# Performance work log

Measured on AMD Instinct MI355X. Metric: run time of the kernel, lower is better.

## Reference

```python
import jax, jax.numpy as jnp
import numpy as np

# NOTE: submodules (VecLayerNorm, VecLinear, VecActivation, VNAttention,
# VNCrossAttention, VNDynamicGraphAttention) are not in the provided source;
# they are reconstructed per standard Vector-Neuron (VN) equivariant layers.

B, C, NQ, NV, K, HEADS = 2, 128, 2048, 2048, 16, 8
HID = 4 * C
EPS = 1e-6
NS = 0.2  # LeakyReLU(0.2) slope used by VecActivation


def vec_layernorm(x, gamma, beta):
    # x: [B,C,3,N] -- equivariant LN: normalize per-channel vector norms,
    # LayerNorm the norms over the channel dim, rescale directions.
    n = jnp.sqrt(jnp.sum(x * x, axis=2, keepdims=True) + EPS)  # [B,C,1,N]
    mu = jnp.mean(n, axis=1, keepdims=True)
    var = jnp.var(n, axis=1, keepdims=True)
    ln = (n - mu) / jnp.sqrt(var + EPS) * gamma[None, :, None, None] + beta[None, :, None, None]
    return x / (n + EPS) * ln


def vlin(x, W):
    # VecLinear: bias-free linear over channel dim (equivariance). x: [B,C,3,N]
    return jnp.einsum('oc,bctn->botn', W, x)


def vn_attention(xq, xkv, Wq, Wk, Wv, Wo):
    # Global equivariant multi-head attention; scores from 3D-vector inner products.
    Bq, Cc, _, Nq = xq.shape
    Dh = Cc // HEADS
    q = vlin(xq, Wq).reshape(Bq, HEADS, Dh, 3, Nq)
    k = vlin(xkv, Wk).reshape(Bq, HEADS, Dh, 3, -1)
    vv = vlin(xkv, Wv).reshape(Bq, HEADS, Dh, 3, -1)
    s = jnp.einsum('bhdtn,bhdtm->bhnm', q, k) / np.float32(np.sqrt(3 * Dh))
    a = jax.nn.softmax(s, axis=-1)
    o = jnp.einsum('bhnm,bhdtm->bhdtn', a, vv).reshape(Bq, Cc, 3, Nq)
    return vlin(o, Wo)


def graph_attention(xq, xv, idx, We):
    # Local kNN graph attention: gather neighbor features by idx, build edge
    # features concat(v_j - q_i, q_i) -> VecLinear, softmax-weight over k neighbors.
    Bq, Cc, _, Nq = xq.shape
    vt = jnp.transpose(xv, (0, 3, 2, 1))                 # [B,Nv,3,C]
    nbr = jax.vmap(lambda vb, ib: vb[ib])(vt, idx)       # [B,Nq,k,3,C]
    qt = jnp.transpose(xq, (0, 3, 2, 1))                 # [B,Nq,3,C]
    center = qt[:, :, None, :, :]
    edge = jnp.concatenate([nbr - center, jnp.broadcast_to(center, nbr.shape)], axis=-1)  # [B,Nq,k,3,2C]
    feat = jnp.einsum('oc,bnktc->bnkto', We, edge)        # [B,Nq,k,3,C]
    s = jnp.einsum('bntc,bnktc->bnk', qt, nbr) / np.float32(np.sqrt(3 * Cc))
    a = jax.nn.softmax(s, axis=-1)
    out = jnp.einsum('bnk,bnkto->bnto', a, feat)          # [B,Nq,3,C]
    return jnp.transpose(out, (0, 3, 2, 1))               # [B,C,3,Nq]


def vn_leaky(x, D):
    # VN-LeakyReLU: learned direction d = D x; reflect negative half-space.
    d = vlin(x, D)
    dot = jnp.sum(x * d, axis=2, keepdims=True)
    dsq = jnp.sum(d * d, axis=2, keepdims=True)
    xneg = x - (dot / (dsq + EPS)) * d
    return NS * x + (1.0 - NS) * jnp.where(dot >= 0, x, xneg)


def setup_inputs() -> dict:
    key = jax.random.key(0)
    ks = jax.random.split(key, 24)

    def w(k_, o, i):
        return jax.random.normal(k_, (o, i), jnp.float32) / np.float32(np.sqrt(i))

    inp = {
        'q': jax.random.normal(ks[0], (B, C, 3, NQ), jnp.float32),
        'v': jax.random.normal(ks[1], (B, C, 3, NV), jnp.float32),
        'q_pos': jax.random.normal(ks[2], (B, NQ, 3), jnp.float32),
        'v_pos': jax.random.normal(ks[3], (B, NV, 3), jnp.float32),
        'self_attn_idx': jax.random.randint(ks[4], (B, NQ, K), 0, NQ),
        'cross_attn_idx': jax.random.randint(ks[5], (B, NQ, K), 0, NV),
        # VecLayerNorm affine params (norm1, norm2, norm_q, norm_v)
        'g1': jnp.ones((C,), jnp.float32), 'b1': jnp.zeros((C,), jnp.float32),
        'g2': jnp.ones((C,), jnp.float32), 'b2': jnp.zeros((C,), jnp.float32),
        'gq': jnp.ones((C,), jnp.float32), 'bq': jnp.zeros((C,), jnp.float32),
        'gv': jnp.ones((C,), jnp.float32), 'bv': jnp.zeros((C,), jnp.float32),
        # self attention (global VN attn + local graph attn + concat merge)
        'Wq_s': w(ks[6], C, C), 'Wk_s': w(ks[7], C, C), 'Wv_s': w(ks[8], C, C), 'Wo_s': w(ks[9], C, C),
        'We_s': w(ks[10], C, 2 * C), 'Wm_s': w(ks[11], C, 2 * C),
        # cross attention
        'Wq_c': w(ks[12], C, C), 'Wk_c': w(ks[13], C, C), 'Wv_c': w(ks[14], C, C), 'Wo_c': w(ks[15], C, C),
        'We_c': w(ks[16], C, 2 * C), 'Wm_c': w(ks[17], C, 2 * C),
        # MLP: VecLinear(C->4C) -> VN-LeakyReLU -> VecLinear(4C->C)
        'W1': w(ks[18], HID, C), 'Dact': w(ks[19], HID, HID), 'W2': w(ks[20], C, HID),
    }
    return inp


def reference(q, v, q_pos, v_pos, self_attn_idx, cross_attn_idx,
              g1, b1, g2, b2, gq, bq, gv, bv,
              Wq_s, Wk_s, Wv_s, Wo_s, We_s, Wm_s,
              Wq_c, Wk_c, Wv_c, Wo_c, We_c, Wm_c,
              W1, Dact, W2):
    # --- self-attention block (norm1 -> global attn + kNN graph attn -> merge -> residual)
    nx = vec_layernorm(q, g1, b1)
    f1 = vn_attention(nx, nx, Wq_s, Wk_s, Wv_s, Wo_s)
    f2 = graph_attention(nx, nx, self_attn_idx, We_s)
    q = q + vlin(jnp.concatenate([f1, f2], axis=1), Wm_s)
    # --- cross-attention block (norm_q / norm_v -> global cross attn + kNN cross graph attn -> merge -> residual)
    nq = vec_layernorm(q, gq, bq)
    nv = vec_layernorm(v, gv, bv)
    f1 = vn_attention(nq, nv, Wq_c, Wk_c, Wv_c, Wo_c)
    f2 = graph_attention(nq, nv, cross_attn_idx, We_c)
    q = q + vlin(jnp.concatenate([f1, f2], axis=1), Wm_c)
    # --- equivariant MLP (norm2 -> VecLinear -> VN-LeakyReLU -> VecLinear -> residual)
    nx = vec_layernorm(q, g2, b2)
    h = vn_leaky(vlin(nx, W1), Dact)
    q = q + vlin(h, W2)
    return q
```

## Files before the change

### kernel.cpp

```cpp
#include <hip/hip_runtime.h>
#include <math.h>

#define B_    2
#define C_    128
#define N_    2048
#define HID_  512
#define HEADS_ 8
#define EPS_  1e-6f
#define NS_   0.2f
#define KSPLIT 8

typedef __attribute__((ext_vector_type(8))) short short8v;
typedef __attribute__((ext_vector_type(4))) float f32x4;
typedef unsigned short ush;
typedef unsigned int u32;

__device__ inline ush f2bf(float f) {
    unsigned u = __float_as_uint(f);
    u += 0x7FFF + ((u >> 16) & 1);
    return (ush)(u >> 16);
}
__device__ inline float bf2f(ush u) { return __uint_as_float((u32)u << 16); }

__device__ inline u32 splitpack(float x) {
    ush hi = f2bf(x);
    float hf = __uint_as_float((u32)hi << 16);
    ush lo = f2bf(x - hf);
    return ((u32)hi << 16) | (u32)lo;
}

__device__ inline void unpack_hi(const u32* buf, short8v& h0, short8v& h1) {
    ush h[16];
    #pragma unroll
    for (int j = 0; j < 16; ++j) h[j] = (ush)(buf[j] >> 16);
    h0 = *(short8v*)&h[0]; h1 = *(short8v*)&h[8];
}

struct LNArgs {
    const float* x[2]; const float* g[2]; const float* bt[2]; ush* ysp[2];
};
__global__ __launch_bounds__(256) void ln_kernel(LNArgs a)
{
    __shared__ float norms[128][32];
    __shared__ float red1[8][32];
    __shared__ float red2[8][32];
    const int s = blockIdx.z;
    const float* x = a.x[s];
    const float* gma = a.g[s];
    const float* bta = a.bt[s];
    ush* ysp = a.ysp[s];

    const int b  = blockIdx.y;
    const int n0 = blockIdx.x * 32;
    const int nn = threadIdx.x & 31;
    const int cg = threadIdx.x >> 5;

    float s1 = 0.f, s2 = 0.f;
    for (int it = 0; it < 16; ++it) {
        int c = it * 8 + cg;
        size_t base = ((size_t)(b * C_ + c) * 3) * N_ + n0 + nn;
        float x0 = x[base], x1 = x[base + N_], x2 = x[base + 2 * N_];
        float nr = sqrtf(x0 * x0 + x1 * x1 + x2 * x2 + EPS_);
        norms[c][nn] = nr;
        s1 += nr; s2 += nr * nr;
    }
    red1[cg][nn] = s1; red2[cg][nn] = s2;
    __syncthreads();
    float S1 = 0.f, S2 = 0.f;
    #pragma unroll
    for (int g = 0; g < 8; ++g) { S1 += red1[g][nn]; S2 += red2[g][nn]; }
    float mu   = S1 * (1.f / 128.f);
    float var  = S2 * (1.f / 128.f) - mu * mu;
    float rstd = rsqrtf(var + EPS_);

    for (int it = 0; it < 16; ++it) {
        int c = it * 8 + cg;
        float nr = norms[c][nn];
        float ln = (nr - mu) * rstd * gma[c] + bta[c];
        float sc = ln / (nr + EPS_);
        size_t base = ((size_t)(b * C_ + c) * 3) * N_ + n0 + nn;
        ysp[base]          = f2bf(x[base] * sc);
        ysp[base + N_]     = f2bf(x[base + N_] * sc);
        ysp[base + 2 * N_] = f2bf(x[base + 2 * N_] * sc);
    }
}

struct WCArgs { const float* src[9]; u32* dst[9]; int n[9]; float scale[9]; };
__global__ __launch_bounds__(256) void wconv_kernel(WCArgs a)
{
    const int w = blockIdx.y;
    const int i = blockIdx.x * 256 + threadIdx.x;
    if (i < a.n[w]) a.dst[w][i] = splitpack(a.src[w][i] * a.scale[w]);
}

struct WFArgs {
    const float* Wm[2]; const float* Wo[2]; const float* We[2];
    u32* Wfa[2]; u32* Wfb[2];
};
__global__ __launch_bounds__(256) void wfuse_kernel(WFArgs a)
{
    const int tg = blockIdx.x * 256 + threadIdx.x;
    const int p = tg / 49152;
    const int rem = tg % 49152;
    if (rem < 16384) {
        const int o = rem >> 7, k = rem & 127;
        const float* Wm = a.Wm[p];
        const float* Wo = a.Wo[p];
        float acc = 0.f;
        #pragma unroll 4
        for (int c = 0; c < 128; ++c)
            acc += Wm[o * 256 + c] * Wo[c * 128 + k];
        a.Wfa[p][o * 128 + k] = splitpack(acc);
    } else {
        const int r2 = rem - 16384;
        const int o = r2 >> 8, k = r2 & 255;
        const float* Wm = a.Wm[p];
        const float* We = a.We[p];
        float acc = 0.f;
        #pragma unroll 4
        for (int c = 0; c < 128; ++c)
            acc += Wm[o * 256 + 128 + c] * We[c * 256 + k];
        a.Wfb[p][o * 256 + k] = splitpack(acc);
    }
}

template <int XMODE, int OMODE, bool XBF>
__device__ __forceinline__ void gemm_tile(
    const u32* __restrict__ Wsp, int wstride,
    const void* __restrict__ Xv, int K,
    const float* __restrict__ Z, float* __restrict__ Y,
    ush* __restrict__ Ybf, ush* __restrict__ Ytr,
    int b, int m0, int o0loc, int oglob, int Ostr,
    ush (*Wh)[64], ush (*Xh)[64])
{
    const int M = 3 * N_;
    const int tid = threadIdx.x;
    const int lane = tid & 63, wv = tid >> 6;
    const int col = lane & 15, grp = lane >> 4;
    const int wo = wv >> 1, wm = wv & 1;

    f32x4 acc[2][2];
    #pragma unroll
    for (int i = 0; i < 2; ++i)
        #pragma unroll
        for (int j = 0; j < 2; ++j) { f32x4 z = {0.f,0.f,0.f,0.f}; acc[i][j] = z; }

    for (int kk = 0; kk < K; kk += 64) {
        {
            const int o = tid >> 2, kg = tid & 3;
            const u32* src = Wsp + (size_t)(o0loc + o) * wstride + kk + kg * 16;
            u32 buf[16];
            #pragma unroll
            for (int j = 0; j < 4; ++j) *(uint4*)&buf[j * 4] = *(const uint4*)(src + j * 4);
            const int s0 = ((kg * 2)     ^ (o & 7)) << 3;
            const int s1 = ((kg * 2 + 1) ^ (o & 7)) << 3;
            short8v h0, h1; unpack_hi(buf, h0, h1);
            *(short8v*)&Wh[o][s0] = h0; *(short8v*)&Wh[o][s1] = h1;
        }
        if (XMODE == 0) {
            const int m = lane, kq = wv;
            const int s0 = ((kq * 2)     ^ (m & 7)) << 3;
            const int s1 = ((kq * 2 + 1) ^ (m & 7)) << 3;
            if (XBF) {
                const ush* src = (const ush*)Xv + ((size_t)b * K + kk + kq * 16) * M + m0 + m;
                ush h[16];
                #pragma unroll
                for (int j = 0; j < 16; ++j) h[j] = src[(size_t)j * M];
                *(short8v*)&Xh[m][s0] = *(short8v*)&h[0];
                *(short8v*)&Xh[m][s1] = *(short8v*)&h[8];
            } else {
                const u32* src = (const u32*)Xv + ((size_t)b * K + kk + kq * 16) * M + m0 + m;
                u32 buf[16];
                #pragma unroll
                for (int j = 0; j < 16; ++j) buf[j] = src[(size_t)j * M];
                short8v h0, h1; unpack_hi(buf, h0, h1);
                *(short8v*)&Xh[m][s0] = h0; *(short8v*)&Xh[m][s1] = h1;
            }
        } else {
            const int m = tid >> 2, kg = tid & 3;
            const int mg = m0 + m;
            const int n = mg & (N_ - 1), t = mg >> 11;
            const int s0 = ((kg * 2)     ^ (m & 7)) << 3;
            const int s1 = ((kg * 2 + 1) ^ (m & 7)) << 3;
            const ush* src = (const ush*)Xv + ((size_t)(b * N_ + n) * 3 + t) * K + kk + kg * 16;
            ush h[16];
            *(uint4*)&h[0] = *(const uint4*)(src);
            *(uint4*)&h[8] = *(const uint4*)(src + 8);
            *(short8v*)&Xh[m][s0] = *(short8v*)&h[0];
            *(short8v*)&Xh[m][s1] = *(short8v*)&h[8];
        }
        __syncthreads();
        #pragma unroll
        for (int kc = 0; kc < 2; ++kc) {
            const int sk = ((kc * 4 + grp) ^ (col & 7)) << 3;
            short8v ah0 = *(const short8v*)&Wh[wo * 32 + col][sk];
            short8v ah1 = *(const short8v*)&Wh[wo * 32 + 16 + col][sk];
            short8v xh0 = *(const short8v*)&Xh[wm * 32 + col][sk];
            short8v xh1 = *(const short8v*)&Xh[wm * 32 + 16 + col][sk];
            acc[0][0] = __builtin_amdgcn_mfma_f32_16x16x32_bf16(ah0, xh0, acc[0][0], 0, 0, 0);
            acc[0][1] = __builtin_amdgcn_mfma_f32_16x16x32_bf16(ah0, xh1, acc[0][1], 0, 0, 0);
            acc[1][0] = __builtin_amdgcn_mfma_f32_16x16x32_bf16(ah1, xh0, acc[1][0], 0, 0, 0);
            acc[1][1] = __builtin_amdgcn_mfma_f32_16x16x32_bf16(ah1, xh1, acc[1][1], 0, 0, 0);
        }
        __syncthreads();
    }
    #pragma unroll
    for (int of = 0; of < 2; ++of) {
        #pragma unroll
        for (int r = 0; r < 4; ++r) {
            const int o = oglob + wo * 32 + of * 16 + grp * 4 + r;
            #pragma unroll
            for (int mf = 0; mf < 2; ++mf) {
                const int mloc = m0 + wm * 32 + mf * 16 + col;
                const size_t idx = ((size_t)b * Ostr + o) * M + mloc;
                float v = acc[of][mf][r];
                if (OMODE == 0 || OMODE == 5) {
                    if (Z) v += Z[idx];
                    Y[idx] = v;
                }
                if (OMODE == 3 || OMODE == 5) Ybf[idx] = f2bf(v);
                if (OMODE == 4) {
                    ush bv = f2bf(v);
                    const int t = mloc >> 11, n = mloc & (N_ - 1);
                    const int h = (o >> 4) & 7, cl = o & 15;
                    const int d = cl * 3 + t;
                    if (o >= 256) {
                        const int kt = n >> 6, hh = (n >> 5) & 1, db = d >> 4;
                        const size_t idx2 = ((size_t)(b * 8 + h) * 192
                                           + (kt * 2 + hh) * 3 + db) * 512
                                          + (((n >> 3) & 3) * 16 + (d & 15)) * 8 + (n & 7);
                        Ybf[idx2] = bv;
                    } else {
                        const int isK = (o >> 7) & 1;
                        const int qg = n >> 4, half = d >> 5;
                        const size_t idx2 = ((size_t)(isK * 16 + b * 8 + h) * 256
                                           + qg * 2 + half) * 512
                                          + (((d >> 3) & 3) * 16 + (n & 15)) * 8 + (d & 7);
                        Ytr[idx2] = bv;
                    }
                }
            }
        }
    }
}

template <int XMODE, int OMODE, bool XBF>
__global__ __launch_bounds__(256) void gemm_kernel2(
    const u32* __restrict__ Wsp, int wstride,
    const void* __restrict__ Xv,
    const float* __restrict__ Z,
    float* __restrict__ Y, ush* __restrict__ Ybf,
    int Ostr, int obase, int K)
{
    __shared__ __align__(16) ush Wh[64][64];
    __shared__ __align__(16) ush Xh[64][64];
    gemm_tile<XMODE, OMODE, XBF>(Wsp, wstride, Xv, K, Z, Y, Ybf, nullptr,
                            blockIdx.z, blockIdx.x * 64,
                            blockIdx.y * 64, obase + blockIdx.y * 64, Ostr,
                            Wh, Xh);
}

__global__ __launch_bounds__(256) void wm2_kernel(
    const u32* __restrict__ Wfa, const u32* __restrict__ Wfb,
    const ush* __restrict__ ao, const ush* __restrict__ gb,
    const float* __restrict__ Z, float* __restrict__ Y)
{
    __shared__ __align__(16) ush Wh[64][64];
    __shared__ __align__(16) ush Xh[64][64];
    const int M = 3 * N_;
    const int b = blockIdx.z;
    const int m0 = blockIdx.x * 64;
    const int o0 = blockIdx.y * 64;
    const int tid = threadIdx.x;
    const int lane = tid & 63, wv = tid >> 6;
    const int col = lane & 15, grp = lane >> 4;
    const int wo = wv >> 1, wm = wv & 1;

    f32x4 acc[2][2];
    #pragma unroll
    for (int i = 0; i < 2; ++i)
        #pragma unroll
        for (int j = 0; j < 2; ++j) { f32x4 z = {0.f,0.f,0.f,0.f}; acc[i][j] = z; }

    for (int kk = 0; kk < 128; kk += 64) {
        {
            const int o = tid >> 2, kg = tid & 3;
            const u32* src = Wfa + (size_t)(o0 + o) * 128 + kk + kg * 16;
            u32 buf[16];
            #pragma unroll
            for (int j = 0; j < 4; ++j) *(uint4*)&buf[j * 4] = *(const uint4*)(src + j * 4);
            const int s0 = ((kg * 2)     ^ (o & 7)) << 3;
            const int s1 = ((kg * 2 + 1) ^ (o & 7)) << 3;
            short8v h0, h1; unpack_hi(buf, h0, h1);
            *(short8v*)&Wh[o][s0] = h0; *(short8v*)&Wh[o][s1] = h1;
        }
        {
            const int m = lane, kq = wv;
            const int s0 = ((kq * 2)     ^ (m & 7)) << 3;
            const int s1 = ((kq * 2 + 1) ^ (m & 7)) << 3;
            const ush* src = ao + ((size_t)b * 128 + kk + kq * 16) * M + m0 + m;
            ush h[16];
            #pragma unroll
            for (int j = 0; j < 16; ++j) h[j] = src[(size_t)j * M];
            *(short8v*)&Xh[m][s0] = *(short8v*)&h[0];
            *(short8v*)&Xh[m][s1] = *(short8v*)&h[8];
        }
        __syncthreads();
        #pragma unroll
        for (int kc = 0; kc < 2; ++kc) {
            const int sk = ((kc * 4 + grp) ^ (col & 7)) << 3;
            short8v ah0 = *(const short8v*)&Wh[wo * 32 + col][sk];
            short8v ah1 = *(const short8v*)&Wh[wo * 32 + 16 + col][sk];
            short8v xh0 = *(const short8v*)&Xh[wm * 32 + col][sk];
            short8v xh1 = *(const short8v*)&Xh[wm * 32 + 16 + col][sk];
            acc[0][0] = __builtin_amdgcn_mfma_f32_16x16x32_bf16(ah0, xh0, acc[0][0], 0, 0, 0);
            acc[0][1] = __builtin_amdgcn_mfma_f32_16x16x32_bf16(ah0, xh1, acc[0][1], 0, 0, 0);
            acc[1][0] = __builtin_amdgcn_mfma_f32_16x16x32_bf16(ah1, xh0, acc[1][0], 0, 0, 0);
            acc[1][1] = __builtin_amdgcn_mfma_f32_16x16x32_bf16(ah1, xh1, acc[1][1], 0, 0, 0);
        }
        __syncthreads();
    }

    for (int kk = 0; kk < 256; kk += 64) {
        {
            const int o = tid >> 2, kg = tid & 3;
            const u32* src = Wfb + (size_t)(o0 + o) * 256 + kk + kg * 16;
            u32 buf[16];
            #pragma unroll
            for (int j = 0; j < 4; ++j) *(uint4*)&buf[j * 4] = *(const uint4*)(src + j * 4);
            const int s0 = ((kg * 2)     ^ (o & 7)) << 3;
            const int s1 = ((kg * 2 + 1) ^ (o & 7)) << 3;
            short8v h0, h1; unpack_hi(buf, h0, h1);
            *(short8v*)&Wh[o][s0] = h0; *(short8v*)&Wh[o][s1] = h1;
        }
        {
            const int m = tid >> 2, kg = tid & 3;
            const int mg = m0 + m;
            const int n = mg & (N_ - 1), t = mg >> 11;
            const int s0 = ((kg * 2)     ^ (m & 7)) << 3;
            const int s1 = ((kg * 2 + 1) ^ (m & 7)) << 3;
            const ush* src = gb + ((size_t)(b * N_ + n) * 3 + t) * 256 + kk + kg * 16;
            ush h[16];
            *(uint4*)&h[0] = *(const uint4*)(src);
            *(uint4*)&h[8] = *(const uint4*)(src + 8);
            *(short8v*)&Xh[m][s0] = *(short8v*)&h[0];
            *(short8v*)&Xh[m][s1] = *(short8v*)&h[8];
        }
        __syncthreads();
        #pragma unroll
        for (int kc = 0; kc < 2; ++kc) {
            const int sk = ((kc * 4 + grp) ^ (col & 7)) << 3;
            short8v ah0 = *(const short8v*)&Wh[wo * 32 + col][sk];
            short8v ah1 = *(const short8v*)&Wh[wo * 32 + 16 + col][sk];
            short8v xh0 = *(const short8v*)&Xh[wm * 32 + col][sk];
            short8v xh1 = *(const short8v*)&Xh[wm * 32 + 16 + col][sk];
            acc[0][0] = __builtin_amdgcn_mfma_f32_16x16x32_bf16(ah0, xh0, acc[0][0], 0, 0, 0);
            acc[0][1] = __builtin_amdgcn_mfma_f32_16x16x32_bf16(ah0, xh1, acc[0][1], 0, 0, 0);
            acc[1][0] = __builtin_amdgcn_mfma_f32_16x16x32_bf16(ah1, xh0, acc[1][0], 0, 0, 0);
            acc[1][1] = __builtin_amdgcn_mfma_f32_16x16x32_bf16(ah1, xh1, acc[1][1], 0, 0, 0);
        }
        __syncthreads();
    }

    #pragma unroll
    for (int of = 0; of < 2; ++of) {
        #pragma unroll
        for (int r = 0; r < 4; ++r) {
            const int o = o0 + wo * 32 + of * 16 + grp * 4 + r;
            #pragma unroll
            for (int mf = 0; mf < 2; ++mf) {
                const int mloc = m0 + wm * 32 + mf * 16 + col;
                const size_t idx = ((size_t)b * 128 + o) * M + mloc;
                Y[idx] = acc[of][mf][r] + Z[idx];
            }
        }
    }
}

struct QKVArgs {
    const u32* W0; const u32* W1; const u32* W2;
    const ush* X0; const ush* X1; const ush* X2;
};

__global__ __launch_bounds__(256) void qkv_tr_kernel(QKVArgs A,
        ush* __restrict__ vfm, ush* __restrict__ qktb,
        const ush* __restrict__ ts0, ush* __restrict__ td0,
        const ush* __restrict__ ts1, ush* __restrict__ td1)
{
    __shared__ __align__(16) ush Wh[64][64];
    __shared__ __align__(16) ush Xh[64][64];
    __shared__ ush ttile[32][34];
    const int bx = blockIdx.x;
    if (bx < 1152) {
        const int z = bx / 576, rem = bx % 576;
        const int y = rem / 96, x = rem % 96;
        const int wi = y >> 1;
        const u32* W = wi == 0 ? A.W0 : (wi == 1 ? A.W1 : A.W2);
        const ush* X = wi == 0 ? A.X0 : (wi == 1 ? A.X1 : A.X2);
        gemm_tile<0, 4, true>(W, 128, X, 128, nullptr, nullptr, vfm, qktb,
                        z, x * 64, (y & 1) * 64, y * 64, 384,
                        Wh, Xh);
    } else {
        int i = bx - 1152;
        const int which = i / 1536; i %= 1536;
        const ush* src = which ? ts1 : ts0;
        ush* dst = which ? td1 : td0;
        const int x = i & 63, y = (i >> 6) & 3, z = i >> 8;
        const int b = z / 3, t = z % 3;
        const int n0 = x * 32, c0 = y * 32;
        const int tx = threadIdx.x & 31, ty = threadIdx.x >> 5;
        #pragma unroll
        for (int p = 0; p < 4; ++p) {
            int c = c0 + ty + p * 8;
            ttile[ty + p * 8][tx] = src[((size_t)(b * C_ + c) * 3 + t) * N_ + n0 + tx];
        }
        __syncthreads();
        #pragma unroll
        for (int p = 0; p < 4; ++p) {
            int n = n0 + ty + p * 8;
            dst[((size_t)(b * N_ + n) * 3 + t) * C_ + c0 + tx] = ttile[tx][ty + p * 8];
        }
    }
}

__global__ __launch_bounds__(256) void attn_mfma_kernel(
    const ush* __restrict__ vfm, const ush* __restrict__ qktb,
    ush* __restrict__ pacc, float* __restrict__ pml)
{
    __shared__ __align__(16) ush Pl[4][2][16][64];

    const int flat = blockIdx.x;
    const int xcd  = flat & 7;
    const int slot = flat >> 3;
    const int gid  = xcd * 4 + (slot >> 6);
    const int q32  = slot & 63;
    const int bh   = gid & 15;
    const int zz   = gid >> 4;

    const int tid = threadIdx.x;
    const int lane = tid & 63, wv = tid >> 6;
    const int col = lane & 15, grp = lane >> 4;
    const int c7  = col & 7;
    const int kz  = zz * 4 + wv;
    const int ks0 = kz * (N_ / KSPLIT);

    const ush* Qpl = qktb + (size_t)bh * 131072;
    const ush* Kpl = qktb + (size_t)(16 + bh) * 131072;
    const ush* Vpl = vfm  + (size_t)bh * 98304;

    short8v qf[2][2];
    #pragma unroll
    for (int qi = 0; qi < 2; ++qi) {
        const int qg = q32 * 2 + qi;
        qf[qi][0] = *(const short8v*)(Qpl + ((size_t)qg * 2 + 0) * 512 + lane * 8);
        qf[qi][1] = *(const short8v*)(Qpl + ((size_t)qg * 2 + 1) * 512 + lane * 8);
    }

    f32x4 acc[2][3];
    #pragma unroll
    for (int qi = 0; qi < 2; ++qi)
        #pragma unroll
        for (int db = 0; db < 3; ++db) { f32x4 z = {0.f,0.f,0.f,0.f}; acc[qi][db] = z; }
    float m_i[2] = {0.f, 0.f};
    float l_l[2] = {0.f, 0.f};

    const int NT = (N_ / KSPLIT) / 64;
    for (int mt = 0; mt < NT; ++mt) {
        const int m0 = ks0 + mt * 64;

        short8v ka[4][2];
        #pragma unroll
        for (int kb = 0; kb < 4; ++kb) {
            const size_t kg = (m0 >> 4) + kb;
            ka[kb][0] = *(const short8v*)(Kpl + (kg * 2 + 0) * 512 + lane * 8);
            ka[kb][1] = *(const short8v*)(Kpl + (kg * 2 + 1) * 512 + lane * 8);
        }
        const int kt = m0 >> 6;
        short8v vf[2][3];
        #pragma unroll
        for (int hh = 0; hh < 2; ++hh)
            #pragma unroll
            for (int db = 0; db < 3; ++db)
                vf[hh][db] = *(const short8v*)(Vpl + (size_t)((kt * 2 + hh) * 3 + db) * 512 + lane * 8);

        f32x4 sf[2][4];
        __builtin_amdgcn_s_setprio(1);
        #pragma unroll
        for (int qi = 0; qi < 2; ++qi)
            #pragma unroll
            for (int kb = 0; kb < 4; ++kb) {
                f32x4 z = {0.f, 0.f, 0.f, 0.f};
                z = __builtin_amdgcn_mfma_f32_16x16x32_bf16(ka[kb][0], qf[qi][0], z, 0, 0, 0);
                z = __builtin_amdgcn_mfma_f32_16x16x32_bf16(ka[kb][1], qf[qi][1], z, 0, 0, 0);
                sf[qi][kb] = z;
            }
        __builtin_amdgcn_s_setprio(0);

        #pragma unroll
        for (int qi = 0; qi < 2; ++qi) {
            float psum = 0.f;
            #pragma unroll
            for (int kb = 0; kb < 4; ++kb) {
                float e0 = __expf(sf[qi][kb][0] - m_i[qi]);
                float e1 = __expf(sf[qi][kb][1] - m_i[qi]);
                float e2 = __expf(sf[qi][kb][2] - m_i[qi]);
                float e3 = __expf(sf[qi][kb][3] - m_i[qi]);
                psum += (e0 + e1) + (e2 + e3);
                u32 r0, r1;
                asm("v_cvt_pk_bf16_f32 %0, %1, %2" : "=v"(r0) : "v"(e0), "v"(e1));
                asm("v_cvt_pk_bf16_f32 %0, %1, %2" : "=v"(r1) : "v"(e2), "v"(e3));
                const int un = (4 * kb + grp) ^ (c7 << 1);
                uint2 pk2; pk2.x = r0; pk2.y = r1;
                *(uint2*)&Pl[wv][qi][col][un << 2] = pk2;
            }
            l_l[qi] += psum;
        }

        __builtin_amdgcn_s_setprio(1);
        #pragma unroll
        for (int qi = 0; qi < 2; ++qi)
            #pragma unroll
            for (int hh = 0; hh < 2; ++hh) {
                const int ur = (8 * hh + 2 * grp) ^ (c7 << 1);
                short8v pf = *(const short8v*)&Pl[wv][qi][col][ur << 2];
                #pragma unroll
                for (int db = 0; db < 3; ++db)
                    acc[qi][db] = __builtin_amdgcn_mfma_f32_16x16x32_bf16(vf[hh][db], pf, acc[qi][db], 0, 0, 0);
            }
        __builtin_amdgcn_s_setprio(0);

        #pragma unroll
        for (int qi = 0; qi < 2; ++qi) {
            float pmax = -1e30f;
            #pragma unroll
            for (int kb = 0; kb < 4; ++kb)
                #pragma unroll
                for (int r = 0; r < 4; ++r) pmax = fmaxf(pmax, sf[qi][kb][r]);
            pmax = fmaxf(pmax, __shfl_xor(pmax, 16, 64));
            pmax = fmaxf(pmax, __shfl_xor(pmax, 32, 64));
            if (!__all(pmax - m_i[qi] <= 8.0f)) {
                float mnew = fmaxf(m_i[qi], pmax);
                float sc = __expf(m_i[qi] - mnew);
                l_l[qi] *= sc;
                #pragma unroll
                for (int db = 0; db < 3; ++db) {
                    acc[qi][db][0] *= sc; acc[qi][db][1] *= sc;
                    acc[qi][db][2] *= sc; acc[qi][db][3] *= sc;
                }
                m_i[qi] = mnew;
            }
        }
    }

    const int ntile = q32 >> 1, qh = q32 & 1;
    const size_t pb = (size_t)(kz * 16 + bh) * 32 + ntile;
    #pragma unroll
    for (int qi = 0; qi < 2; ++qi) {
        float l = l_l[qi];
        l += __shfl_xor(l, 16, 64);
        l += __shfl_xor(l, 32, 64);
        const int q = qh * 32 + qi * 16 + col;
        #pragma unroll
        for (int db = 0; db < 3; ++db)
            #pragma unroll
            for (int r = 0; r < 4; ++r) {
                int d = db * 16 + grp * 4 + r;
                pacc[pb * 3072 + d * 64 + q] = f2bf(acc[qi][db][r]);
            }
        if (grp == 0) {
            pml[pb * 128 + q]      = m_i[qi];
            pml[pb * 128 + 64 + q] = l;
        }
    }
}

__global__ __launch_bounds__(256) void graph_kernel(
    const ush* __restrict__ tq, const ush* __restrict__ tv,
    const int* __restrict__ idx, ush* __restrict__ gbuf)
{
    __shared__ float centerf[384];
    __shared__ ush nbr_l[16][384];
    __shared__ float sd[16];
    __shared__ int nbr_i[16];
    const int b = blockIdx.y, n = blockIdx.x;
    const int tid = threadIdx.x;
    const ush* qrow = tq + (size_t)(b * N_ + n) * 384;
    for (int e = tid; e < 384; e += 256) centerf[e] = bf2f(qrow[e]);
    if (tid < 16) nbr_i[tid] = idx[(size_t)(b * N_ + n) * 16 + tid];
    __syncthreads();

    const int lane = tid & 63, wv = tid >> 6;
    for (int kk = 0; kk < 4; ++kk) {
        int k = wv * 4 + kk;
        const u32* vrow = (const u32*)(tv + ((size_t)b * N_ + nbr_i[k]) * 384);
        float p = 0.f;
        #pragma unroll
        for (int jj = 0; jj < 3; ++jj) {
            int e2 = lane + jj * 64;
            u32 v2 = vrow[e2];
            ((u32*)nbr_l[k])[e2] = v2;
            p += centerf[e2 * 2]     * bf2f((ush)(v2 & 0xffff))
               + centerf[e2 * 2 + 1] * bf2f((ush)(v2 >> 16));
        }
        #pragma unroll
        for (int off = 32; off; off >>= 1) p += __shfl_down(p, off, 64);
        if (lane == 0) sd[k] = p * 0.05103103630798288f;
    }
    __syncthreads();

    float mx = -1e30f;
    #pragma unroll
    for (int k = 0; k < 16; ++k) mx = fmaxf(mx, sd[k]);
    float a[16]; float ssum = 0.f;
    #pragma unroll
    for (int k = 0; k < 16; ++k) { a[k] = __expf(sd[k] - mx); ssum += a[k]; }
    float inv = 1.f / ssum;

    for (int e = tid; e < 384; e += 256) {
        float accv = 0.f;
        #pragma unroll
        for (int k = 0; k < 16; ++k)
            accv += a[k] * bf2f(nbr_l[k][e]);
        accv *= inv;
        float ce = centerf[e];
        int t = e >> 7, c = e & 127;
        size_t gb = ((size_t)(b * N_ + n) * 3 + t) * 256;
        gbuf[gb + c]       = f2bf(accv - ce);
        gbuf[gb + 128 + c] = f2bf(ce);
    }
}

__global__ __launch_bounds__(256) void attn_reduce_kernel(
    const ush* __restrict__ pacc, const float* __restrict__ pml,
    ush* __restrict__ ao)
{
    const int nt = blockIdx.x, bh = blockIdx.y;
    const int b = bh >> 3, h = bh & 7;
    const int tid = threadIdx.x;
    const int q = tid & 63, dg = tid >> 6;

    size_t pb[KSPLIT];
    float m[KSPLIT], l[KSPLIT];
    #pragma unroll
    for (int kz = 0; kz < KSPLIT; ++kz) {
        pb[kz] = (size_t)(kz * 16 + bh) * 32 + nt;
        m[kz] = pml[pb[kz] * 128 + q];
        l[kz] = pml[pb[kz] * 128 + 64 + q];
    }
    float ms = -1e30f;
    #pragma unroll
    for (int kz = 0; kz < KSPLIT; ++kz) ms = fmaxf(ms, m[kz]);
    float w[KSPLIT], ls = 0.f;
    #pragma unroll
    for (int kz = 0; kz < KSPLIT; ++kz) { w[kz] = __expf(m[kz] - ms); ls += l[kz] * w[kz]; }
    const float inv = 1.f / ls;

    const size_t hb = ((size_t)(b * C_ + h * 16)) * 3 * N_;
    #pragma unroll
    for (int j = 0; j < 12; ++j) {
        int d = dg * 12 + j;
        float o = 0.f;
        #pragma unroll
        for (int kz = 0; kz < KSPLIT; ++kz)
            o += bf2f(pacc[pb[kz] * 3072 + d * 64 + q]) * w[kz];
        ao[hb + (size_t)d * N_ + nt * 64 + q] = f2bf(o * inv);
    }
}

__global__ __launch_bounds__(256) void leaky_kernel(const float* __restrict__ x,
                                                    const float* __restrict__ d,
                                                    ush* __restrict__ y)
{
    size_t p = (size_t)blockIdx.x * 256 + threadIdx.x;
    size_t bh = p / N_, n = p % N_;
    size_t base = bh * 3 * N_ + n;
    float x0 = x[base], x1 = x[base + N_], x2 = x[base + 2 * N_];
    float d0 = d[base], d1 = d[base + N_], d2 = d[base + 2 * N_];
    float dot = x0 * d0 + x1 * d1 + x2 * d2;
    float dsq = d0 * d0 + d1 * d1 + d2 * d2;
    float f = dot / (dsq + EPS_);
    bool pos = dot >= 0.f;
    float y0 = pos ? x0 : x0 - f * d0;
    float y1 = pos ? x1 : x1 - f * d1;
    float y2 = pos ? x2 : x2 - f * d2;
    y[base]          = f2bf(NS_ * x0 + (1.f - NS_) * y0);
    y[base + N_]     = f2bf(NS_ * x1 + (1.f - NS_) * y1);
    y[base + 2 * N_] = f2bf(NS_ * x2 + (1.f - NS_) * y2);
}

extern "C" void kernel_launch(void* const* d_in, const int* in_sizes, int n_in,
                              void* d_out, int out_size, void* d_ws, size_t ws_size,
                              hipStream_t stream)
{
    const float* q_in = (const float*)d_in[0];
    const float* v_in = (const float*)d_in[1];
    const int*   idx_s = (const int*)d_in[4];
    const int*   idx_c = (const int*)d_in[5];
    const float* g1 = (const float*)d_in[6];
    const float* b1 = (const float*)d_in[7];
    const float* g2 = (const float*)d_in[8];
    const float* b2 = (const float*)d_in[9];
    const float* gq = (const float*)d_in[10];
    const float* bq = (const float*)d_in[11];
    const float* gv = (const float*)d_in[12];
    const float* bv = (const float*)d_in[13];
    float* out = (float*)d_out;
    float* ws  = (float*)d_ws;

    const size_t S1 = (size_t)B_ * C_ * 3 * N_;
    ush*   nx_b  = (ush*)(ws + 2*S1);
    ush*   nv_b  = (ush*)(ws + 3*S1);
    ush*   vfm   = (ush*)(ws + 4*S1);
    ush*   qktb  = (ush*)(ws + 5*S1) + S1;
    ush*   ao_b  = (ush*)(ws + 7*S1);
    ush*   gbuf_b= (ush*)(ws + 8*S1);
    float* qa    = ws + 12*S1;
    float* qb    = ws + 13*S1;
    ush*   t1_b  = (ush*)(ws + 14*S1);
    ush*   t2_b  = (ush*)(ws + 15*S1);
    u32*   wsp   = (u32*)(ws + 16*S1);
    ush*   pacc  = (ush*)(ws + 8*S1);
    float* pml   = (float*)(ws + 2*S1);
    float* hd    = ws;
    float* h1    = ws + 4*S1;
    ush*   h1_b  = (ush*)(ws + 14*S1);
    ush*   h1_b2 = (ush*)(ws + 8*S1);

    const int wn[9]   = {16384,16384,16384, 16384,16384,16384, 65536,262144,65536};
    const int wsrc[9] = {14,15,16, 20,21,22, 26,27,28};
    u32* wd[9];
    {
        int off = 0;
        for (int i = 0; i < 9; ++i) { wd[i] = wsp + off; off += wn[i]; }
    }
    u32 *Wq_s = wd[0], *Wk_s = wd[1], *Wv_s = wd[2];
    u32 *Wq_c = wd[3], *Wk_c = wd[4], *Wv_c = wd[5];
    u32 *W1 = wd[6], *Dact = wd[7], *W2 = wd[8];
    u32* Wfa_s = wsp + 491520;
    u32* Wfb_s = Wfa_s + 16384;
    u32* Wfa_c = Wfb_s + 32768;
    u32* Wfb_c = Wfa_c + 16384;

    hipMemsetAsync(qktb, 0, (size_t)32 * 131072 * sizeof(ush), stream);

    {
        WCArgs a;
        for (int i = 0; i < 9; ++i) {
            a.src[i] = (const float*)d_in[wsrc[i]];
            a.dst[i] = wd[i];
            a.n[i]   = wn[i];
            a.scale[i] = 1.f;
        }
        a.scale[0] = 0.14433756729740643f;
        a.scale[3] = 0.14433756729740643f;
        wconv_kernel<<<dim3(1024, 9), 256, 0, stream>>>(a);
    }
    {
        WFArgs a;
        a.Wm[0] = (const float*)d_in[19]; a.Wo[0] = (const float*)d_in[17]; a.We[0] = (const float*)d_in[18];
        a.Wm[1] = (const float*)d_in[25]; a.Wo[1] = (const float*)d_in[23]; a.We[1] = (const float*)d_in[24];
        a.Wfa[0] = Wfa_s; a.Wfb[0] = Wfb_s;
        a.Wfa[1] = Wfa_c; a.Wfb[1] = Wfb_c;
        wfuse_kernel<<<dim3(384), 256, 0, stream>>>(a);
    }

    dim3 gar(N_ / 64, B_ * HEADS_);
    dim3 ggr(N_, B_);
    dim3 gwm(96, 2, B_);
    dim3 gg512(96, 8, B_);

    {
        LNArgs la{};
        la.x[0] = q_in; la.g[0] = g1; la.bt[0] = b1; la.ysp[0] = nx_b;
        ln_kernel<<<dim3(64, B_, 1), 256, 0, stream>>>(la);
    }
    {
        QKVArgs A{Wq_s, Wk_s, Wv_s, nx_b, nx_b, nx_b};
        qkv_tr_kernel<<<dim3(1152 + 1536), 256, 0, stream>>>(A, vfm, qktb, nx_b, t1_b, nullptr, nullptr);
    }
    attn_mfma_kernel<<<dim3(2048), 256, 0, stream>>>(vfm, qktb, pacc, pml);
    attn_reduce_kernel<<<gar, 256, 0, stream>>>(pacc, pml, ao_b);
    graph_kernel<<<ggr, 256, 0, stream>>>(t1_b, t1_b, idx_s, gbuf_b);
    wm2_kernel<<<gwm, 256, 0, stream>>>(Wfa_s, Wfb_s, ao_b, gbuf_b, q_in, qa);

    {
        LNArgs la{};
        la.x[0] = qa;   la.g[0] = gq; la.bt[0] = bq; la.ysp[0] = nx_b;
        la.x[1] = v_in; la.g[1] = gv; la.bt[1] = bv; la.ysp[1] = nv_b;
        ln_kernel<<<dim3(64, B_, 2), 256, 0, stream>>>(la);
    }
    {
        QKVArgs A{Wq_c, Wk_c, Wv_c, nx_b, nv_b, nv_b};
        qkv_tr_kernel<<<dim3(1152 + 3072), 256, 0, stream>>>(A, vfm, qktb, nx_b, t1_b, nv_b, t2_b);
    }
    attn_mfma_kernel<<<dim3(2048), 256, 0, stream>>>(vfm, qktb, pacc, pml);
    attn_reduce_kernel<<<gar, 256, 0, stream>>>(pacc, pml, ao_b);
    graph_kernel<<<ggr, 256, 0, stream>>>(t1_b, t2_b, idx_c, gbuf_b);
    wm2_kernel<<<gwm, 256, 0, stream>>>(Wfa_c, Wfb_c, ao_b, gbuf_b, qa, qb);

    {
        LNArgs la{};
        la.x[0] = qb; la.g[0] = g2; la.bt[0] = b2; la.ysp[0] = nx_b;
        ln_kernel<<<dim3(64, B_, 1), 256, 0, stream>>>(la);
    }
    gemm_kernel2<0,5,true><<<gg512, 256, 0, stream>>>(W1, 128, nx_b, nullptr, h1, h1_b, 512, 0, 128);
    gemm_kernel2<0,0,true><<<gg512, 256, 0, stream>>>(Dact, 512, h1_b, nullptr, hd, nullptr, 512, 0, 512);
    leaky_kernel<<<dim3((B_ * HID_ * N_) / 256), 256, 0, stream>>>(h1, hd, h1_b2);
    gemm_kernel2<0,0,true><<<dim3(96, 2, B_), 256, 0, stream>>>(W2, 512, h1_b2, qb, out, nullptr, 128, 0, 512);
}
```

Before: 251.6 us.

## Merge attention reduce with graph attention kernel; store MLP intermediates in bf16

Merges the split-K attention reduction and the kNN graph attention into one launch. The first 512 blocks do the reduction and the remaining 4096 blocks do the graph gather, which removes one launch per block and lets the two independent jobs overlap. The MLP's W1 and Dact GEMM outputs are now written only as bf16, so the fp32 copies are gone and the leaky activation reads bf16 inputs, cutting memory traffic. Workspace buffers are reassigned to match (gbuf moves to offset 0, hd_b to 1*S1). The cost is slightly lower precision for the inputs to the activation.

```diff
diff --git a/kernel.cpp b/kernel.cpp
--- a/kernel.cpp
+++ b/kernel.cpp
@@ -214,11 +214,11 @@
                 const int mloc = m0 + wm * 32 + mf * 16 + col;
                 const size_t idx = ((size_t)b * Ostr + o) * M + mloc;
                 float v = acc[of][mf][r];
-                if (OMODE == 0 || OMODE == 5) {
+                if (OMODE == 0) {
                     if (Z) v += Z[idx];
                     Y[idx] = v;
                 }
-                if (OMODE == 3 || OMODE == 5) Ybf[idx] = f2bf(v);
+                if (OMODE == 3) Ybf[idx] = f2bf(v);
                 if (OMODE == 4) {
                     ush bv = f2bf(v);
                     const int t = mloc >> 11, n = mloc & (N_ - 1);
@@ -574,7 +574,9 @@
     }
 }
 
-__global__ __launch_bounds__(256) void graph_kernel(
+__global__ __launch_bounds__(256) void reduce_graph_kernel(
+    const ush* __restrict__ pacc, const float* __restrict__ pml,
+    ush* __restrict__ ao,
     const ush* __restrict__ tq, const ush* __restrict__ tv,
     const int* __restrict__ idx, ush* __restrict__ gbuf)
 {
@@ -582,100 +584,98 @@
     __shared__ ush nbr_l[16][384];
     __shared__ float sd[16];
     __shared__ int nbr_i[16];
-    const int b = blockIdx.y, n = blockIdx.x;
     const int tid = threadIdx.x;
-    const ush* qrow = tq + (size_t)(b * N_ + n) * 384;
-    for (int e = tid; e < 384; e += 256) centerf[e] = bf2f(qrow[e]);
-    if (tid < 16) nbr_i[tid] = idx[(size_t)(b * N_ + n) * 16 + tid];
-    __syncthreads();
-
-    const int lane = tid & 63, wv = tid >> 6;
-    for (int kk = 0; kk < 4; ++kk) {
-        int k = wv * 4 + kk;
-        const u32* vrow = (const u32*)(tv + ((size_t)b * N_ + nbr_i[k]) * 384);
-        float p = 0.f;
-        #pragma unroll
-        for (int jj = 0; jj < 3; ++jj) {
-            int e2 = lane + jj * 64;
-            u32 v2 = vrow[e2];
-            ((u32*)nbr_l[k])[e2] = v2;
-            p += centerf[e2 * 2]     * bf2f((ush)(v2 & 0xffff))
-               + centerf[e2 * 2 + 1] * bf2f((ush)(v2 >> 16));
-        }
-        #pragma unroll
-        for (int off = 32; off; off >>= 1) p += __shfl_down(p, off, 64);
-        if (lane == 0) sd[k] = p * 0.05103103630798288f;
-    }
-    __syncthreads();
-
-    float mx = -1e30f;
-    #pragma unroll
-    for (int k = 0; k < 16; ++k) mx = fmaxf(mx, sd[k]);
-    float a[16]; float ssum = 0.f;
-    #pragma unroll
-    for (int k = 0; k < 16; ++k) { a[k] = __expf(sd[k] - mx); ssum += a[k]; }
-    float inv = 1.f / ssum;
-
-    for (int e = tid; e < 384; e += 256) {
-        float accv = 0.f;
-        #pragma unroll
-        for (int k = 0; k < 16; ++k)
-            accv += a[k] * bf2f(nbr_l[k][e]);
-        accv *= inv;
-        float ce = centerf[e];
-        int t = e >> 7, c = e & 127;
-        size_t gb = ((size_t)(b * N_ + n) * 3 + t) * 256;
-        gbuf[gb + c]       = f2bf(accv - ce);
-        gbuf[gb + 128 + c] = f2bf(ce);
-    }
-}
-
-__global__ __launch_bounds__(256) void attn_reduce_kernel(
-    const ush* __restrict__ pacc, const float* __restrict__ pml,
-    ush* __restrict__ ao)
-{
-    const int nt = blockIdx.x, bh = blockIdx.y;
-    const int b = bh >> 3, h = bh & 7;
-    const int tid = threadIdx.x;
-    const int q = tid & 63, dg = tid >> 6;
-
-    size_t pb[KSPLIT];
-    float m[KSPLIT], l[KSPLIT];
-    #pragma unroll
-    for (int kz = 0; kz < KSPLIT; ++kz) {
-        pb[kz] = (size_t)(kz * 16 + bh) * 32 + nt;
-        m[kz] = pml[pb[kz] * 128 + q];
-        l[kz] = pml[pb[kz] * 128 + 64 + q];
-    }
-    float ms = -1e30f;
-    #pragma unroll
-    for (int kz = 0; kz < KSPLIT; ++kz) ms = fmaxf(ms, m[kz]);
-    float w[KSPLIT], ls = 0.f;
-    #pragma unroll
-    for (int kz = 0; kz < KSPLIT; ++kz) { w[kz] = __expf(m[kz] - ms); ls += l[kz] * w[kz]; }
-    const float inv = 1.f / ls;
-
-    const size_t hb = ((size_t)(b * C_ + h * 16)) * 3 * N_;
-    #pragma unroll
-    for (int j = 0; j < 12; ++j) {
-        int d = dg * 12 + j;
-        float o = 0.f;
-        #pragma unroll
-        for (int kz = 0; kz < KSPLIT; ++kz)
-            o += bf2f(pacc[pb[kz] * 3072 + d * 64 + q]) * w[kz];
-        ao[hb + (size_t)d * N_ + nt * 64 + q] = f2bf(o * inv);
-    }
-}
-
-__global__ __launch_bounds__(256) void leaky_kernel(const float* __restrict__ x,
-                                                    const float* __restrict__ d,
+
+    if (blockIdx.x < 512) {
+        const int nt = blockIdx.x & 31, bh = blockIdx.x >> 5;
+        const int b = bh >> 3, h = bh & 7;
+        const int q = tid & 63, dg = tid >> 6;
+
+        size_t pb[KSPLIT];
+        float m[KSPLIT], l[KSPLIT];
+        #pragma unroll
+        for (int kz = 0; kz < KSPLIT; ++kz) {
+            pb[kz] = (size_t)(kz * 16 + bh) * 32 + nt;
+            m[kz] = pml[pb[kz] * 128 + q];
+            l[kz] = pml[pb[kz] * 128 + 64 + q];
+        }
+        float ms = -1e30f;
+        #pragma unroll
+        for (int kz = 0; kz < KSPLIT; ++kz) ms = fmaxf(ms, m[kz]);
+        float w[KSPLIT], ls = 0.f;
+        #pragma unroll
+        for (int kz = 0; kz < KSPLIT; ++kz) { w[kz] = __expf(m[kz] - ms); ls += l[kz] * w[kz]; }
+        const float inv = 1.f / ls;
+
+        const size_t hb = ((size_t)(b * C_ + h * 16)) * 3 * N_;
+        #pragma unroll
+        for (int j = 0; j < 12; ++j) {
+            int d = dg * 12 + j;
+            float o = 0.f;
+            #pragma unroll
+            for (int kz = 0; kz < KSPLIT; ++kz)
+                o += bf2f(pacc[pb[kz] * 3072 + d * 64 + q]) * w[kz];
+            ao[hb + (size_t)d * N_ + nt * 64 + q] = f2bf(o * inv);
+        }
+    } else {
+        const int j = blockIdx.x - 512;
+        const int b = j >> 11, n = j & 2047;
+        const ush* qrow = tq + (size_t)(b * N_ + n) * 384;
+        for (int e = tid; e < 384; e += 256) centerf[e] = bf2f(qrow[e]);
+        if (tid < 16) nbr_i[tid] = idx[(size_t)(b * N_ + n) * 16 + tid];
+        __syncthreads();
+
+        const int lane = tid & 63, wv = tid >> 6;
+        for (int kk = 0; kk < 4; ++kk) {
+            int k = wv * 4 + kk;
+            const u32* vrow = (const u32*)(tv + ((size_t)b * N_ + nbr_i[k]) * 384);
+            float p = 0.f;
+            #pragma unroll
+            for (int jj = 0; jj < 3; ++jj) {
+                int e2 = lane + jj * 64;
+                u32 v2 = vrow[e2];
+                ((u32*)nbr_l[k])[e2] = v2;
+                p += centerf[e2 * 2]     * bf2f((ush)(v2 & 0xffff))
+                   + centerf[e2 * 2 + 1] * bf2f((ush)(v2 >> 16));
+            }
+            #pragma unroll
+            for (int off = 32; off; off >>= 1) p += __shfl_down(p, off, 64);
+            if (lane == 0) sd[k] = p * 0.05103103630798288f;
+        }
+        __syncthreads();
+
+        float mx = -1e30f;
+        #pragma unroll
+        for (int k = 0; k < 16; ++k) mx = fmaxf(mx, sd[k]);
+        float a[16]; float ssum = 0.f;
+        #pragma unroll
+        for (int k = 0; k < 16; ++k) { a[k] = __expf(sd[k] - mx); ssum += a[k]; }
+        float inv = 1.f / ssum;
+
+        for (int e = tid; e < 384; e += 256) {
+            float accv = 0.f;
+            #pragma unroll
+            for (int k = 0; k < 16; ++k)
+                accv += a[k] * bf2f(nbr_l[k][e]);
+            accv *= inv;
+            float ce = centerf[e];
+            int t = e >> 7, c = e & 127;
+            size_t gb = ((size_t)(b * N_ + n) * 3 + t) * 256;
+            gbuf[gb + c]       = f2bf(accv - ce);
+            gbuf[gb + 128 + c] = f2bf(ce);
+        }
+    }
+}
+
+__global__ __launch_bounds__(256) void leaky_kernel(const ush* __restrict__ x,
+                                                    const ush* __restrict__ d,
                                                     ush* __restrict__ y)
 {
     size_t p = (size_t)blockIdx.x * 256 + threadIdx.x;
     size_t bh = p / N_, n = p % N_;
     size_t base = bh * 3 * N_ + n;
-    float x0 = x[base], x1 = x[base + N_], x2 = x[base + 2 * N_];
-    float d0 = d[base], d1 = d[base + N_], d2 = d[base + 2 * N_];
+    float x0 = bf2f(x[base]), x1 = bf2f(x[base + N_]), x2 = bf2f(x[base + 2 * N_]);
+    float d0 = bf2f(d[base]), d1 = bf2f(d[base + N_]), d2 = bf2f(d[base + 2 * N_]);
     float dot = x0 * d0 + x1 * d1 + x2 * d2;
     float dsq = d0 * d0 + d1 * d1 + d2 * d2;
     float f = dot / (dsq + EPS_);
@@ -708,12 +708,12 @@
     float* ws  = (float*)d_ws;
 
     const size_t S1 = (size_t)B_ * C_ * 3 * N_;
+    ush*   gbuf_b= (ush*)(ws);
     ush*   nx_b  = (ush*)(ws + 2*S1);
     ush*   nv_b  = (ush*)(ws + 3*S1);
     ush*   vfm   = (ush*)(ws + 4*S1);
     ush*   qktb  = (ush*)(ws + 5*S1) + S1;
     ush*   ao_b  = (ush*)(ws + 7*S1);
-    ush*   gbuf_b= (ush*)(ws + 8*S1);
     float* qa    = ws + 12*S1;
     float* qb    = ws + 13*S1;
     ush*   t1_b  = (ush*)(ws + 14*S1);
@@ -721,8 +721,7 @@
     u32*   wsp   = (u32*)(ws + 16*S1);
     ush*   pacc  = (ush*)(ws + 8*S1);
     float* pml   = (float*)(ws + 2*S1);
-    float* hd    = ws;
-    float* h1    = ws + 4*S1;
+    ush*   hd_b  = (ush*)(ws + 1*S1);
     ush*   h1_b  = (ush*)(ws + 14*S1);
     ush*   h1_b2 = (ush*)(ws + 8*S1);
 
@@ -764,8 +763,6 @@
         wfuse_kernel<<<dim3(384), 256, 0, stream>>>(a);
     }
 
-    dim3 gar(N_ / 64, B_ * HEADS_);
-    dim3 ggr(N_, B_);
     dim3 gwm(96, 2, B_);
     dim3 gg512(96, 8, B_);
 
@@ -779,8 +776,7 @@
         qkv_tr_kernel<<<dim3(1152 + 1536), 256, 0, stream>>>(A, vfm, qktb, nx_b, t1_b, nullptr, nullptr);
     }
     attn_mfma_kernel<<<dim3(2048), 256, 0, stream>>>(vfm, qktb, pacc, pml);
-    attn_reduce_kernel<<<gar, 256, 0, stream>>>(pacc, pml, ao_b);
-    graph_kernel<<<ggr, 256, 0, stream>>>(t1_b, t1_b, idx_s, gbuf_b);
+    reduce_graph_kernel<<<dim3(512 + 4096), 256, 0, stream>>>(pacc, pml, ao_b, t1_b, t1_b, idx_s, gbuf_b);
     wm2_kernel<<<gwm, 256, 0, stream>>>(Wfa_s, Wfb_s, ao_b, gbuf_b, q_in, qa);
 
     {
@@ -794,8 +790,7 @@
         qkv_tr_kernel<<<dim3(1152 + 3072), 256, 0, stream>>>(A, vfm, qktb, nx_b, t1_b, nv_b, t2_b);
     }
     attn_mfma_kernel<<<dim3(2048), 256, 0, stream>>>(vfm, qktb, pacc, pml);
-    attn_reduce_kernel<<<gar, 256, 0, stream>>>(pacc, pml, ao_b);
-    graph_kernel<<<ggr, 256, 0, stream>>>(t1_b, t2_b, idx_c, gbuf_b);
+    reduce_graph_kernel<<<dim3(512 + 4096), 256, 0, stream>>>(pacc, pml, ao_b, t1_b, t2_b, idx_c, gbuf_b);
     wm2_kernel<<<gwm, 256, 0, stream>>>(Wfa_c, Wfb_c, ao_b, gbuf_b, qa, qb);
 
     {
@@ -803,8 +798,8 @@
         la.x[0] = qb; la.g[0] = g2; la.bt[0] = b2; la.ysp[0] = nx_b;
         ln_kernel<<<dim3(64, B_, 1), 256, 0, stream>>>(la);
     }
-    gemm_kernel2<0,5,true><<<gg512, 256, 0, stream>>>(W1, 128, nx_b, nullptr, h1, h1_b, 512, 0, 128);
-    gemm_kernel2<0,0,true><<<gg512, 256, 0, stream>>>(Dact, 512, h1_b, nullptr, hd, nullptr, 512, 0, 512);
-    leaky_kernel<<<dim3((B_ * HID_ * N_) / 256), 256, 0, stream>>>(h1, hd, h1_b2);
+    gemm_kernel2<0,3,true><<<gg512, 256, 0, stream>>>(W1, 128, nx_b, nullptr, nullptr, h1_b, 512, 0, 128);
+    gemm_kernel2<0,3,true><<<gg512, 256, 0, stream>>>(Dact, 512, h1_b, nullptr, nullptr, hd_b, 512, 0, 512);
+    leaky_kernel<<<dim3((B_ * HID_ * N_) / 256), 256, 0, stream>>>(h1_b, hd_b, h1_b2);
     gemm_kernel2<0,0,true><<<dim3(96, 2, B_), 256, 0, stream>>>(W2, 512, h1_b2, qb, out, nullptr, 128, 0, 512);
 }
```

Result: faster. 239.2 us (-4.9%).
